# Performance work log

Hardware: AMD Instinct MI355X
Metric: run time of the kernel (lower is better)

The kernel has to match this reference:

```python
import jax, jax.numpy as jnp
import numpy as np

HEAD_DIM = 128
NUM_HEADS = 16
NUM_KV_HEADS = 16
ROPE_MAX_POS = 4096
ROPE_BASE = 10000.0


def _rope_tables(seq_len):
    # cos/sin cached tables: [S, D/2]
    inv_freq = 1.0 / (ROPE_BASE ** (jnp.arange(0, HEAD_DIM, 2, dtype=jnp.float32) / HEAD_DIM))
    t = jnp.arange(seq_len, dtype=jnp.float32)
    freqs = jnp.outer(t, inv_freq)
    return jnp.cos(freqs), jnp.sin(freqs)


def _apply_rope(x, cos, sin):
    # x: [B, S, H, D]; cos/sin: [S, D/2] -> broadcast over heads as [S, 1, D/2]
    orig_dtype = x.dtype
    c = cos[:, None, :]
    s = sin[:, None, :]
    xf = x.astype(jnp.float32)
    x_real, x_im = jnp.split(xf, 2, axis=-1)  # half-split (not interleaved) RoPE
    x_real_e = x_real * c - x_im * s
    x_im_e = x_im * c + x_real * s
    return jnp.concatenate((x_real_e, x_im_e), axis=-1).astype(orig_dtype)


def setup_inputs() -> dict:
    key = jax.random.key(0)
    k1, k2, k3 = jax.random.split(key, 3)
    B, S, H = 1, 4096, 2048
    hidden_states = jax.random.normal(k1, (B, S, H), dtype=jnp.float32)
    # trunc-normal-ish init, std ~ 1/sqrt(fan_in)
    w_qkv = jax.random.normal(k2, ((NUM_HEADS + 2 * NUM_KV_HEADS) * HEAD_DIM, H), dtype=jnp.float32) / jnp.sqrt(jnp.float32(H))
    w_o = jax.random.normal(k3, (H, NUM_HEADS * HEAD_DIM), dtype=jnp.float32) / jnp.sqrt(jnp.float32(NUM_HEADS * HEAD_DIM))
    return {"hidden_states": hidden_states, "w_qkv": w_qkv, "w_o": w_o}


def reference(hidden_states, w_qkv, w_o):
    B, S, _ = hidden_states.shape
    qkv = jnp.einsum('bsh,oh->bso', hidden_states, w_qkv)
    qkv = qkv.reshape(B, S, NUM_HEADS + 2 * NUM_KV_HEADS, HEAD_DIM)
    q = qkv[:, :, :NUM_HEADS]
    k = qkv[:, :, NUM_HEADS:NUM_HEADS + NUM_KV_HEADS]
    v = qkv[:, :, NUM_HEADS + NUM_KV_HEADS:]

    cos, sin = _rope_tables(S)
    q = _apply_rope(q, cos, sin)
    k = _apply_rope(k, cos, sin)

    scale = 1.0 / jnp.sqrt(jnp.float32(HEAD_DIM)).astype(q.dtype)
    # scores: [B, H, Sq, Sk]
    scores = jnp.einsum('bqhd,bkhd->bhqk', q, k) * scale
    causal = jnp.tril(jnp.ones((S, S), dtype=bool))
    scores = jnp.where(causal[None, None], scores, jnp.finfo(scores.dtype).min)
    probs = jax.nn.softmax(scores, axis=-1)
    attn = jnp.einsum('bhqk,bkhd->bqhd', probs, v)
    attn = attn.reshape(B, S, NUM_HEADS * HEAD_DIM)
    return jnp.einsum('bso,ho->bsh', attn, w_o)
```

## Files before the change

kernel.cpp:

```cpp
#include <hip/hip_runtime.h>

typedef __bf16 bf16;
typedef __bf16 bf16x8 __attribute__((ext_vector_type(8)));
typedef __bf16 bf16x4 __attribute__((ext_vector_type(4)));
typedef float f32x4 __attribute__((ext_vector_type(4)));

#define SEQ 4096
#define QKV_LD 6144
#define HNUM 16

__device__ __forceinline__ void async16(const bf16* g, bf16* l) {
    __builtin_amdgcn_global_load_lds((const __attribute__((address_space(1))) void*)g,
                                     (__attribute__((address_space(3))) void*)l, 16, 0, 0);
}

__global__ __launch_bounds__(256) void cast_f32_bf16(const float* __restrict__ src,
                                                     bf16* __restrict__ dst, int n) {
    int i = (blockIdx.x * 256 + threadIdx.x) * 8;
    if (i >= n) return;
    f32x4 a = *(const f32x4*)(src + i);
    f32x4 b = *(const f32x4*)(src + i + 4);
    bf16x8 w;
#pragma unroll
    for (int j = 0; j < 4; j++) { w[j] = (bf16)a[j]; w[4 + j] = (bf16)b[j]; }
    *(bf16x8*)(dst + i) = w;
}

template <int A_F32, int B_F32, int C_F32>
__global__ __launch_bounds__(256) void gemm_nt(const void* __restrict__ Ap,
                                               const void* __restrict__ Bp,
                                               void* __restrict__ Cp,
                                               int M, int N, int K) {
    __shared__ __align__(16) bf16 sA[128 * 32];
    __shared__ __align__(16) bf16 sB[128 * 32];
    const int tid  = threadIdx.x;
    const int wave = tid >> 6, lane = tid & 63;
    const int qd = lane >> 4, ln = lane & 15;
    const int bm = blockIdx.x * 128, bn = blockIdx.y * 128;
    const int wm = (wave >> 1) * 64, wn = (wave & 1) * 64;

    const int srow = wave * 16 + (lane >> 2);
    const int scol = (lane & 3) * 8;
    const size_t rowoff = (size_t)srow * K + scol;
    const size_t rowskip = (size_t)64 * K;

    const bf16* Ab = (const bf16*)Ap + (size_t)bm * K + rowoff;
    const bf16* Bb = (const bf16*)Bp + (size_t)bn * K + rowoff;
    const float* Af = (const float*)Ap + (size_t)bm * K + rowoff;
    const float* Bf = (const float*)Bp + (size_t)bn * K + rowoff;
    bf16* sAd0 = &sA[(wave * 16) * 32];
    bf16* sAd1 = &sA[(64 + wave * 16) * 32];
    bf16* sBd0 = &sB[(wave * 16) * 32];
    bf16* sBd1 = &sB[(64 + wave * 16) * 32];
    bf16* sAw0 = &sA[srow * 32 + scol];
    bf16* sAw1 = &sA[(64 + srow) * 32 + scol];
    bf16* sBw0 = &sB[srow * 32 + scol];
    bf16* sBw1 = &sB[(64 + srow) * 32 + scol];

    f32x4 acc[4][4] = {};
    for (int k0 = 0; k0 < K; k0 += 32) {
        if (A_F32) {
            f32x4 u0 = *(const f32x4*)(Af + k0);
            f32x4 u1 = *(const f32x4*)(Af + k0 + 4);
            f32x4 u2 = *(const f32x4*)(Af + rowskip + k0);
            f32x4 u3 = *(const f32x4*)(Af + rowskip + k0 + 4);
            bf16x8 w0, w1;
#pragma unroll
            for (int i = 0; i < 4; i++) { w0[i] = (bf16)u0[i]; w0[4 + i] = (bf16)u1[i];
                                          w1[i] = (bf16)u2[i]; w1[4 + i] = (bf16)u3[i]; }
            *(bf16x8*)sAw0 = w0;
            *(bf16x8*)sAw1 = w1;
        } else {
            async16(Ab + k0, sAd0);
            async16(Ab + rowskip + k0, sAd1);
        }
        if (B_F32) {
            f32x4 u0 = *(const f32x4*)(Bf + k0);
            f32x4 u1 = *(const f32x4*)(Bf + k0 + 4);
            f32x4 u2 = *(const f32x4*)(Bf + rowskip + k0);
            f32x4 u3 = *(const f32x4*)(Bf + rowskip + k0 + 4);
            bf16x8 w0, w1;
#pragma unroll
            for (int i = 0; i < 4; i++) { w0[i] = (bf16)u0[i]; w0[4 + i] = (bf16)u1[i];
                                          w1[i] = (bf16)u2[i]; w1[4 + i] = (bf16)u3[i]; }
            *(bf16x8*)sBw0 = w0;
            *(bf16x8*)sBw1 = w1;
        } else {
            async16(Bb + k0, sBd0);
            async16(Bb + rowskip + k0, sBd1);
        }
        __syncthreads();
        bf16x8 af[4], bfr[4];
#pragma unroll
        for (int i = 0; i < 4; i++)
            af[i] = *(const bf16x8*)&sA[(wm + i * 16 + ln) * 32 + qd * 8];
#pragma unroll
        for (int j = 0; j < 4; j++)
            bfr[j] = *(const bf16x8*)&sB[(wn + j * 16 + ln) * 32 + qd * 8];
#pragma unroll
        for (int i = 0; i < 4; i++)
#pragma unroll
            for (int j = 0; j < 4; j++)
                acc[i][j] = __builtin_amdgcn_mfma_f32_16x16x32_bf16(af[i], bfr[j], acc[i][j], 0, 0, 0);
        __syncthreads();
    }
    const size_t cbase = (size_t)(bm + wm + qd * 4) * N + (bn + wn + ln);
#pragma unroll
    for (int i = 0; i < 4; i++)
#pragma unroll
        for (int j = 0; j < 4; j++)
#pragma unroll
            for (int r = 0; r < 4; r++) {
                size_t idx = cbase + (size_t)(i * 16 + r) * N + j * 16;
                if (C_F32) ((float*)Cp)[idx] = acc[i][j][r];
                else       ((bf16*)Cp)[idx] = (bf16)acc[i][j][r];
            }
}

__global__ __launch_bounds__(256) void rope_k(bf16* __restrict__ QKV) {
    const int s  = blockIdx.x;
    const int t  = threadIdx.x;
    const int hh = (blockIdx.y << 2) + (t >> 6);
    const int d  = t & 63;
    bf16* p = QKV + (size_t)s * QKV_LD + hh * 128 + d;
    float x0 = (float)p[0];
    float x1 = (float)p[64];
    float inv_freq = powf(10000.0f, -(float)d * (1.0f / 64.0f));
    float ang = (float)s * inv_freq;
    float c = cosf(ang), sn = sinf(ang);
    p[0]  = (bf16)(x0 * c - x1 * sn);
    p[64] = (bf16)(x1 * c + x0 * sn);
}

__global__ __launch_bounds__(256, 2) void flash_attn(const bf16* __restrict__ QKV,
                                                     bf16* __restrict__ O) {
    __shared__ __align__(16) bf16 sK[64 * 128];
    __shared__ __align__(16) bf16 sV[128 * 64];
    __shared__ __align__(16) bf16 sP[4][32 * 64];
    const int tid  = threadIdx.x;
    const int wave = tid >> 6, lane = tid & 63;
    const int qd = lane >> 4, ln = lane & 15;
    const int h  = blockIdx.x;
    const int qtile = 31 - blockIdx.y;
    const int qw0 = qtile * 128 + wave * 32;
    const int nkv = 2 * qtile + 2;
    const float scale = 0.08838834764831843f;

    bf16x8 Qf[2][4];
#pragma unroll
    for (int qt = 0; qt < 2; qt++) {
        const bf16* Qg = QKV + (size_t)(qw0 + qt * 16 + ln) * QKV_LD + h * 128;
#pragma unroll
        for (int ks = 0; ks < 4; ks++) {
            bf16x8 q8 = *(const bf16x8*)(Qg + ks * 32 + qd * 8);
#pragma unroll
            for (int e = 0; e < 8; e++) q8[e] = (bf16)((float)q8[e] * scale);
            Qf[qt][ks] = q8;
        }
    }

    f32x4 Oacc[2][8] = {};
    float l_i[2] = {0.0f, 0.0f};

    const int krow = tid >> 4;
    const int kblk = tid & 15;
    const int vd   = tid & 127;
    const int vh   = tid >> 7;
    const bf16* Kg = QKV + 2048 + h * 128;
    const bf16* Vg = QKV + 4096 + h * 128;

    bf16x8 Kpre[4], Vpre[4];
#pragma unroll
    for (int rr = 0; rr < 4; rr++)
        Kpre[rr] = *(const bf16x8*)(Kg + (size_t)(rr * 16 + krow) * QKV_LD + kblk * 8);
#pragma unroll
    for (int u = 0; u < 4; u++)
#pragma unroll
        for (int j = 0; j < 8; j++)
            Vpre[u][j] = Vg[(size_t)(vh * 32 + u * 8 + j) * QKV_LD + vd];

    for (int kt = 0; kt < nkv; kt++) {
        const int kbase = kt * 64;
#pragma unroll
        for (int rr = 0; rr < 4; rr++) {
            int kv = rr * 16 + krow;
            *(bf16x8*)&sK[kv * 128 + ((kblk ^ (kv & 7)) * 8)] = Kpre[rr];
        }
#pragma unroll
        for (int u = 0; u < 4; u++)
            *(bf16x8*)&sV[vd * 64 + (((vh * 4 + u) ^ (vd & 7)) * 8)] = Vpre[u];
        __syncthreads();
        if (kt + 1 < nkv) {
            const int nb = kbase + 64;
#pragma unroll
            for (int rr = 0; rr < 4; rr++)
                Kpre[rr] = *(const bf16x8*)(Kg + (size_t)(nb + rr * 16 + krow) * QKV_LD + kblk * 8);
#pragma unroll
            for (int u = 0; u < 4; u++)
#pragma unroll
                for (int j = 0; j < 8; j++)
                    Vpre[u][j] = Vg[(size_t)(nb + vh * 32 + u * 8 + j) * QKV_LD + vd];
        }
        if (kbase <= qw0 + 31) {
            f32x4 Sacc[2][4] = {};
#pragma unroll
            for (int ks = 0; ks < 4; ks++)
#pragma unroll
                for (int j = 0; j < 4; j++) {
                    bf16x8 af = *(const bf16x8*)&sK[(j * 16 + ln) * 128 + (((ks * 4 + qd) ^ (ln & 7)) * 8)];
                    Sacc[0][j] = __builtin_amdgcn_mfma_f32_16x16x32_bf16(af, Qf[0][ks], Sacc[0][j], 0, 0, 0);
                    Sacc[1][j] = __builtin_amdgcn_mfma_f32_16x16x32_bf16(af, Qf[1][ks], Sacc[1][j], 0, 0, 0);
                }
#pragma unroll
            for (int qt = 0; qt < 2; qt++) {
                const int qs = qw0 + qt * 16;
                if (kbase + 63 > qs) {
#pragma unroll
                    for (int j = 0; j < 4; j++)
#pragma unroll
                        for (int r = 0; r < 4; r++)
                            if (kbase + j * 16 + qd * 4 + r > qs + ln) Sacc[qt][j][r] = -1e30f;
                }
                float psum = 0.0f;
#pragma unroll
                for (int j = 0; j < 4; j++) {
                    bf16x4 p4;
#pragma unroll
                    for (int r = 0; r < 4; r++) {
                        float p = __expf(Sacc[qt][j][r]);
                        psum += p;
                        p4[r] = (bf16)p;
                    }
                    int blk = (j * 2 + (qd >> 1)) ^ (ln & 7);
                    *(bf16x4*)&sP[wave][(qt * 16 + ln) * 64 + blk * 8 + (qd & 1) * 4] = p4;
                }
                psum += __shfl_xor(psum, 16);
                psum += __shfl_xor(psum, 32);
                l_i[qt] += psum;
            }
#pragma unroll
            for (int ks = 0; ks < 2; ks++) {
                bf16x8 pf0 = *(const bf16x8*)&sP[wave][(0 * 16 + ln) * 64 + (((ks * 4 + qd) ^ (ln & 7)) * 8)];
                bf16x8 pf1 = *(const bf16x8*)&sP[wave][(1 * 16 + ln) * 64 + (((ks * 4 + qd) ^ (ln & 7)) * 8)];
#pragma unroll
                for (int dt = 0; dt < 8; dt++) {
                    bf16x8 vf = *(const bf16x8*)&sV[(dt * 16 + ln) * 64 + (((ks * 4 + qd) ^ (ln & 7)) * 8)];
                    Oacc[0][dt] = __builtin_amdgcn_mfma_f32_16x16x32_bf16(pf0, vf, Oacc[0][dt], 0, 0, 0);
                    Oacc[1][dt] = __builtin_amdgcn_mfma_f32_16x16x32_bf16(pf1, vf, Oacc[1][dt], 0, 0, 0);
                }
            }
        }
        __syncthreads();
    }
#pragma unroll
    for (int qt = 0; qt < 2; qt++) {
        float linv[4];
#pragma unroll
        for (int r = 0; r < 4; r++)
            linv[r] = 1.0f / __shfl(l_i[qt], (lane & 48) | (qd * 4 + r));
        bf16* Ob = O + (size_t)(qw0 + qt * 16 + qd * 4) * 2048 + h * 128 + ln;
#pragma unroll
        for (int dt = 0; dt < 8; dt++)
#pragma unroll
            for (int r = 0; r < 4; r++)
                Ob[(size_t)r * 2048 + dt * 16] = (bf16)(Oacc[qt][dt][r] * linv[r]);
    }
}

extern "C" void kernel_launch(void* const* d_in, const int* in_sizes, int n_in,
                              void* d_out, int out_size, void* d_ws, size_t ws_size,
                              hipStream_t stream) {
    const float* X    = (const float*)d_in[0];
    const float* Wqkv = (const float*)d_in[1];
    const float* Wo   = (const float*)d_in[2];
    float* out = (float*)d_out;
    bf16* QKV = (bf16*)d_ws;
    bf16* ATT = QKV + (size_t)4096 * 6144;

    const size_t nX = (size_t)4096 * 2048, nWq = (size_t)6144 * 2048, nWo = (size_t)2048 * 2048;
    const size_t need = (nX * 3 + nWq * 2 + nWo) * 2 + nX * 2;

    if (ws_size >= need) {
        bf16* Xb  = ATT + nX;
        bf16* Wqb = Xb + nX;
        bf16* Wob = Wqb + nWq;
        cast_f32_bf16<<<(int)(nX  / 8 / 256), 256, 0, stream>>>(X, Xb, (int)nX);
        cast_f32_bf16<<<(int)(nWq / 8 / 256), 256, 0, stream>>>(Wqkv, Wqb, (int)nWq);
        cast_f32_bf16<<<(int)(nWo / 8 / 256), 256, 0, stream>>>(Wo, Wob, (int)nWo);
        gemm_nt<0, 0, 0><<<dim3(32, 48), 256, 0, stream>>>(Xb, Wqb, QKV, 4096, 6144, 2048);
        rope_k<<<dim3(4096, 8), 256, 0, stream>>>(QKV);
        flash_attn<<<dim3(HNUM, 32), 256, 0, stream>>>(QKV, ATT);
        gemm_nt<0, 0, 1><<<dim3(32, 16), 256, 0, stream>>>(ATT, Wob, out, 4096, 2048, 2048);
    } else {
        gemm_nt<1, 1, 0><<<dim3(32, 48), 256, 0, stream>>>(X, Wqkv, QKV, 4096, 6144, 2048);
        rope_k<<<dim3(4096, 8), 256, 0, stream>>>(QKV);
        flash_attn<<<dim3(HNUM, 32), 256, 0, stream>>>(QKV, ATT);
        gemm_nt<0, 1, 1><<<dim3(32, 16), 256, 0, stream>>>(ATT, Wo, out, 4096, 2048, 2048);
    }
}
```

Baseline: 494.7 us.

## Pre-transpose V for coalesced attention loads and tabulate RoPE cos/sin

Adds a transpose kernel that writes V as [head*dim, seq] into the freed X buffer, so flash attention can load V tiles with 16-byte vector loads instead of scalar strided gathers. Adds a precomputed cos/sin table, stored in the freed bf16 weight buffer, so the RoPE kernel reads table entries instead of calling powf, cosf and sinf for every element. The cost is two extra kernel launches and an extra write and read pass over V. The fallback path for small workspaces keeps the old behaviour.

```diff
diff --git a/kernel.cpp b/kernel.cpp
--- a/kernel.cpp
+++ b/kernel.cpp
@@ -117,7 +117,30 @@
             }
 }
 
-__global__ __launch_bounds__(256) void rope_k(bf16* __restrict__ QKV) {
+__global__ __launch_bounds__(256) void rope_table(float* __restrict__ T) {
+    int i = blockIdx.x * 256 + threadIdx.x;
+    int s = i >> 6, d = i & 63;
+    float inv_freq = powf(10000.0f, -(float)d * (1.0f / 64.0f));
+    float ang = (float)s * inv_freq;
+    T[2 * i]     = cosf(ang);
+    T[2 * i + 1] = sinf(ang);
+}
+
+__global__ __launch_bounds__(256) void rope_k_tab(bf16* __restrict__ QKV,
+                                                  const float* __restrict__ T) {
+    const int s  = blockIdx.x;
+    const int t  = threadIdx.x;
+    const int hh = (blockIdx.y << 2) + (t >> 6);
+    const int d  = t & 63;
+    bf16* p = QKV + (size_t)s * QKV_LD + hh * 128 + d;
+    float2 cs = ((const float2*)T)[(size_t)s * 64 + d];
+    float x0 = (float)p[0];
+    float x1 = (float)p[64];
+    p[0]  = (bf16)(x0 * cs.x - x1 * cs.y);
+    p[64] = (bf16)(x1 * cs.x + x0 * cs.y);
+}
+
+__global__ __launch_bounds__(256) void rope_k_inline(bf16* __restrict__ QKV) {
     const int s  = blockIdx.x;
     const int t  = threadIdx.x;
     const int hh = (blockIdx.y << 2) + (t >> 6);
@@ -132,7 +155,31 @@
     p[64] = (bf16)(x1 * c + x0 * sn);
 }
 
+__global__ __launch_bounds__(256) void transpose_v(const bf16* __restrict__ QKV,
+                                                   bf16* __restrict__ VT) {
+    __shared__ bf16 t[64][65];
+    const int s0 = blockIdx.x * 64;
+    const int d0 = blockIdx.y * 64;
+    const int r = threadIdx.x >> 3, c = threadIdx.x & 7;
+#pragma unroll
+    for (int u = 0; u < 2; u++) {
+        bf16x8 v = *(const bf16x8*)(QKV + (size_t)(s0 + u * 32 + r) * QKV_LD + 4096 + d0 + c * 8);
+#pragma unroll
+        for (int e = 0; e < 8; e++) t[u * 32 + r][c * 8 + e] = v[e];
+    }
+    __syncthreads();
+#pragma unroll
+    for (int u = 0; u < 2; u++) {
+        bf16x8 w;
+#pragma unroll
+        for (int e = 0; e < 8; e++) w[e] = t[c * 8 + e][u * 32 + r];
+        *(bf16x8*)(VT + (size_t)(d0 + u * 32 + r) * SEQ + s0 + c * 8) = w;
+    }
+}
+
+template <int USE_VT>
 __global__ __launch_bounds__(256, 2) void flash_attn(const bf16* __restrict__ QKV,
+                                                     const bf16* __restrict__ VT,
                                                      bf16* __restrict__ O) {
     __shared__ __align__(16) bf16 sK[64 * 128];
     __shared__ __align__(16) bf16 sV[128 * 64];
@@ -164,20 +211,29 @@
 
     const int krow = tid >> 4;
     const int kblk = tid & 15;
+    const int vrow = tid >> 3;
+    const int vblk = tid & 7;
     const int vd   = tid & 127;
     const int vh   = tid >> 7;
-    const bf16* Kg = QKV + 2048 + h * 128;
-    const bf16* Vg = QKV + 4096 + h * 128;
+    const bf16* Kg  = QKV + 2048 + h * 128;
+    const bf16* Vg  = QKV + 4096 + h * 128;
+    const bf16* VTg = VT + (size_t)h * 128 * SEQ;
 
     bf16x8 Kpre[4], Vpre[4];
 #pragma unroll
     for (int rr = 0; rr < 4; rr++)
         Kpre[rr] = *(const bf16x8*)(Kg + (size_t)(rr * 16 + krow) * QKV_LD + kblk * 8);
-#pragma unroll
-    for (int u = 0; u < 4; u++)
-#pragma unroll
-        for (int j = 0; j < 8; j++)
-            Vpre[u][j] = Vg[(size_t)(vh * 32 + u * 8 + j) * QKV_LD + vd];
+    if (USE_VT) {
+#pragma unroll
+        for (int u = 0; u < 4; u++)
+            Vpre[u] = *(const bf16x8*)(VTg + (size_t)(u * 32 + vrow) * SEQ + vblk * 8);
+    } else {
+#pragma unroll
+        for (int u = 0; u < 4; u++)
+#pragma unroll
+            for (int j = 0; j < 8; j++)
+                Vpre[u][j] = Vg[(size_t)(vh * 32 + u * 8 + j) * QKV_LD + vd];
+    }
 
     for (int kt = 0; kt < nkv; kt++) {
         const int kbase = kt * 64;
@@ -186,20 +242,34 @@
             int kv = rr * 16 + krow;
             *(bf16x8*)&sK[kv * 128 + ((kblk ^ (kv & 7)) * 8)] = Kpre[rr];
         }
-#pragma unroll
-        for (int u = 0; u < 4; u++)
-            *(bf16x8*)&sV[vd * 64 + (((vh * 4 + u) ^ (vd & 7)) * 8)] = Vpre[u];
+        if (USE_VT) {
+#pragma unroll
+            for (int u = 0; u < 4; u++) {
+                int d = u * 32 + vrow;
+                *(bf16x8*)&sV[d * 64 + ((vblk ^ (d & 7)) * 8)] = Vpre[u];
+            }
+        } else {
+#pragma unroll
+            for (int u = 0; u < 4; u++)
+                *(bf16x8*)&sV[vd * 64 + (((vh * 4 + u) ^ (vd & 7)) * 8)] = Vpre[u];
+        }
         __syncthreads();
         if (kt + 1 < nkv) {
             const int nb = kbase + 64;
 #pragma unroll
             for (int rr = 0; rr < 4; rr++)
                 Kpre[rr] = *(const bf16x8*)(Kg + (size_t)(nb + rr * 16 + krow) * QKV_LD + kblk * 8);
-#pragma unroll
-            for (int u = 0; u < 4; u++)
-#pragma unroll
-                for (int j = 0; j < 8; j++)
-                    Vpre[u][j] = Vg[(size_t)(nb + vh * 32 + u * 8 + j) * QKV_LD + vd];
+            if (USE_VT) {
+#pragma unroll
+                for (int u = 0; u < 4; u++)
+                    Vpre[u] = *(const bf16x8*)(VTg + (size_t)(u * 32 + vrow) * SEQ + nb + vblk * 8);
+            } else {
+#pragma unroll
+                for (int u = 0; u < 4; u++)
+#pragma unroll
+                    for (int j = 0; j < 8; j++)
+                        Vpre[u][j] = Vg[(size_t)(nb + vh * 32 + u * 8 + j) * QKV_LD + vd];
+            }
         }
         if (kbase <= qw0 + 31) {
             f32x4 Sacc[2][4] = {};
@@ -284,17 +354,21 @@
         bf16* Xb  = ATT + nX;
         bf16* Wqb = Xb + nX;
         bf16* Wob = Wqb + nWq;
+        bf16*  VT  = Xb;
+        float* Tab = (float*)Wqb;
         cast_f32_bf16<<<(int)(nX  / 8 / 256), 256, 0, stream>>>(X, Xb, (int)nX);
         cast_f32_bf16<<<(int)(nWq / 8 / 256), 256, 0, stream>>>(Wqkv, Wqb, (int)nWq);
         cast_f32_bf16<<<(int)(nWo / 8 / 256), 256, 0, stream>>>(Wo, Wob, (int)nWo);
         gemm_nt<0, 0, 0><<<dim3(32, 48), 256, 0, stream>>>(Xb, Wqb, QKV, 4096, 6144, 2048);
-        rope_k<<<dim3(4096, 8), 256, 0, stream>>>(QKV);
-        flash_attn<<<dim3(HNUM, 32), 256, 0, stream>>>(QKV, ATT);
+        rope_table<<<1024, 256, 0, stream>>>(Tab);
+        rope_k_tab<<<dim3(4096, 8), 256, 0, stream>>>(QKV, Tab);
+        transpose_v<<<dim3(64, 32), 256, 0, stream>>>(QKV, VT);
+        flash_attn<1><<<dim3(HNUM, 32), 256, 0, stream>>>(QKV, VT, ATT);
         gemm_nt<0, 0, 1><<<dim3(32, 16), 256, 0, stream>>>(ATT, Wob, out, 4096, 2048, 2048);
     } else {
         gemm_nt<1, 1, 0><<<dim3(32, 48), 256, 0, stream>>>(X, Wqkv, QKV, 4096, 6144, 2048);
-        rope_k<<<dim3(4096, 8), 256, 0, stream>>>(QKV);
-        flash_attn<<<dim3(HNUM, 32), 256, 0, stream>>>(QKV, ATT);
+        rope_k_inline<<<dim3(4096, 8), 256, 0, stream>>>(QKV);
+        flash_attn<0><<<dim3(HNUM, 32), 256, 0, stream>>>(QKV, (const bf16*)nullptr, ATT);
         gemm_nt<0, 1, 1><<<dim3(32, 16), 256, 0, stream>>>(ATT, Wo, out, 4096, 2048, 2048);
     }
 }
```

Result: faster. 457.5 us (-7.5%).
